# Kernel optimization log

Hardware: AMD Instinct MI355X
Metric: run time of the kernel (lower is better)

The kernel has to match this reference:

```python
import jax, jax.numpy as jnp
import numpy as np

ALPHA = 0.5
INV_COEFF = 25.0
STD_COEFF = 25.0
COV_COEFF = 1.0
NUM_MATCHES = 50
EPS = 1e-5
GAMMA = 1.0


def _cdist(a, b):
    # (B,M,C),(B,N,C) -> (B,M,N) euclidean, matmul-based like torch.cdist
    a2 = jnp.sum(a * a, axis=-1, keepdims=True)            # (B,M,1)
    b2 = jnp.sum(b * b, axis=-1, keepdims=True)            # (B,N,1)
    d2 = a2 + jnp.swapaxes(b2, -1, -2) - 2.0 * jnp.einsum('bmc,bnc->bmn', a, b)
    return jnp.sqrt(jnp.maximum(d2, 0.0))


def _nn_match(input_maps, candidate_maps, distances, num_matches):
    # topk(k=1, largest=False) == min/argmin over last dim
    nn_dists = jnp.min(distances, axis=-1)                 # (B,M)
    nn_indices = jnp.argmin(distances, axis=-1)            # (B,M)
    # k smallest nn_dists, ascending order
    _, best_input_idx = jax.lax.top_k(-nn_dists, num_matches)   # (B,k)
    best_cand_idx = jnp.take_along_axis(nn_indices, best_input_idx, axis=1)
    filt_in = jnp.take_along_axis(input_maps, best_input_idx[:, :, None], axis=1)
    filt_cand = jnp.take_along_axis(candidate_maps, best_cand_idx[:, :, None], axis=1)
    return filt_in, filt_cand


def _off_diag_sq_sum(c):
    return jnp.sum(c * c) - jnp.sum(jnp.diag(c) ** 2)


def _std_term(x_flat):
    # unbiased variance over sample dim (torch var default)
    std = jnp.sqrt(jnp.var(x_flat, axis=0, ddof=1) + EPS)
    return jnp.mean(jax.nn.relu(GAMMA - std)) / 2.0


def _cov_term(x_flat):
    n, c = x_flat.shape
    xc = x_flat - jnp.mean(x_flat, axis=0)
    cov = xc.T @ xc / (n - 1)
    return _off_diag_sq_sum(cov) / c


def _vicreg_global(x, y):
    inv = jnp.mean((x - y) ** 2)
    std = _std_term(x) + _std_term(y)
    cov = _cov_term(x) + _cov_term(y)
    return INV_COEFF * inv + STD_COEFF * std + COV_COEFF * cov


def _vicregl_maps(x, y):
    # x, y: (B, k, C)
    inv = jnp.mean((x - y) ** 2)
    xf = x.reshape(-1, x.shape[-1])
    yf = y.reshape(-1, y.shape[-1])
    std = _std_term(xf) + _std_term(yf)
    cov = _cov_term(xf) + _cov_term(yf)
    return INV_COEFF * inv, STD_COEFF * std, COV_COEFF * cov


def _local_loss(spatial_1, spatial_2):
    B, C, H, W = spatial_1.shape
    maps_1 = spatial_1.reshape(B, C, H * W).transpose(0, 2, 1)   # (B,HW,C)
    maps_2 = spatial_2.reshape(B, C, H * W).transpose(0, 2, 1)
    d12 = _cdist(maps_1, maps_2)
    m1f, m1n = _nn_match(maps_1, maps_2, d12, NUM_MATCHES)
    d21 = _cdist(maps_2, maps_1)
    m2f, m2n = _nn_match(maps_2, maps_1, d21, NUM_MATCHES)
    inv1, var1, cov1 = _vicregl_maps(m1f, m1n)
    inv2, var2, cov2 = _vicregl_maps(m2f, m2n)
    return (inv1 + inv2) / 2 + (var1 + var2) / 2 + (cov1 + cov2) / 2


def setup_inputs() -> dict:
    key = jax.random.key(0)
    k1, k2, k3, k4 = jax.random.split(key, 4)
    B, C, H, W = 64, 768, 24, 24
    return {
        'spatial_1': jax.random.normal(k1, (B, C, H, W), dtype=jnp.float32),
        'pooled_1': jax.random.normal(k2, (B, C), dtype=jnp.float32),
        'spatial_2': jax.random.normal(k3, (B, C, H, W), dtype=jnp.float32),
        'pooled_2': jax.random.normal(k4, (B, C), dtype=jnp.float32),
    }


def reference(spatial_1, pooled_1, spatial_2, pooled_2):
    global_loss = _vicreg_global(pooled_1, pooled_2)
    local_loss = _local_loss(spatial_1, spatial_2)
    return ALPHA * global_loss + (1.0 - ALPHA) * local_loss
```

## Files before the change

### kernel.cpp

```cpp
#include <hip/hip_runtime.h>
#include <stdint.h>

typedef unsigned long long ull;
typedef unsigned int uint;
typedef unsigned short ushort;

typedef __attribute__((ext_vector_type(8))) short short8;
typedef __attribute__((ext_vector_type(4))) float floatx4;

#define B   64
#define C   768
#define HW  576
#define K   50
#define NLOC (B*K)

#define OFF_SLOTS   0
#define OFF_COLSUM  256
#define OFF_NN1     18688
#define OFF_NN2     313600
#define OFF_SELP    608512
#define OFF_SELQ    634112
#define OFF_XT      954624
#define OFF_MP      OFF_XT
#define OFF_XGT     114200832
#define OFF_M       133861632

#define SLOT_INVG 0
#define SLOT_STD  1
#define SLOT_COV  7
#define SLOT_INV1 13
#define SLOT_INV2 14

__device__ __forceinline__ ull umin64(ull a, ull b) { return a < b ? a : b; }

__device__ __forceinline__ float bf2f_lo(uint u) { return __uint_as_float(u << 16); }
__device__ __forceinline__ float bf2f_hi(uint u) { return __uint_as_float(u & 0xffff0000u); }
__device__ __forceinline__ float bf2f(ushort u) { return __uint_as_float(((uint)u) << 16); }

__device__ __forceinline__ ushort f2bf(float f) {
    uint u = __float_as_uint(f);
    uint r = (u + 0x7fffu + ((u >> 16) & 1u)) >> 16;
    return (ushort)r;
}

__device__ __forceinline__ float blk_reduce_sum(float v, float* s4) {
    for (int off = 32; off > 0; off >>= 1) v += __shfl_down(v, off, 64);
    int lane = threadIdx.x & 63, w = threadIdx.x >> 6;
    if (lane == 0) s4[w] = v;
    __syncthreads();
    float r = 0.f;
    if (threadIdx.x == 0) r = s4[0] + s4[1] + s4[2] + s4[3];
    return r;
}

__global__ __launch_bounds__(256) void convert_kernel(const float* __restrict__ x1,
                                                      const float* __restrict__ x2,
                                                      ushort* __restrict__ xT,
                                                      float* __restrict__ normp) {
    int z = blockIdx.y;
    int which = z >> 6, b = z & 63;
    int half = blockIdx.x & 1;
    int pt = blockIdx.x >> 1;
    int p0 = pt * 64, c0 = half * 384;
    const float* X = (which ? x2 : x1) + ((size_t)b * C + c0) * HW + p0;

    __shared__ ushort tile[64][392];
    __shared__ float nlds[64][4];

    int t = threadIdx.x;
    int pq = t & 15, cq = t >> 4;
    int w = t >> 6;

    float ss[4] = {0.f, 0.f, 0.f, 0.f};

#pragma unroll
    for (int pass = 0; pass < 6; ++pass) {
        floatx4 v[4];
#pragma unroll
        for (int i = 0; i < 4; ++i)
            v[i] = *(const floatx4*)(X + (size_t)(pass * 64 + 4 * cq + i) * HW + 4 * pq);
#pragma unroll
        for (int j = 0; j < 4; ++j) {
            ushort u0 = f2bf(v[0][j]), u1 = f2bf(v[1][j]);
            ushort u2 = f2bf(v[2][j]), u3 = f2bf(v[3][j]);
            ushort4 uu; uu.x = u0; uu.y = u1; uu.z = u2; uu.w = u3;
            *(ushort4*)&tile[4 * pq + j][pass * 64 + 4 * cq] = uu;
            float r0 = bf2f(u0), r1 = bf2f(u1), r2 = bf2f(u2), r3 = bf2f(u3);
            ss[j] = fmaf(r0, r0, ss[j]); ss[j] = fmaf(r1, r1, ss[j]);
            ss[j] = fmaf(r2, r2, ss[j]); ss[j] = fmaf(r3, r3, ss[j]);
        }
    }
#pragma unroll
    for (int j = 0; j < 4; ++j) {
        ss[j] += __shfl_xor(ss[j], 16, 64);
        ss[j] += __shfl_xor(ss[j], 32, 64);
    }
    if ((t & 63) < 16) {
#pragma unroll
        for (int j = 0; j < 4; ++j) nlds[4 * pq + j][w] = ss[j];
    }
    __syncthreads();

    ushort* dst = xT + (((size_t)which * B + b) * HW + p0) * C + c0;
    const char* tb = (const char*)tile;
#pragma unroll
    for (int step = 0; step < 12; ++step) {
        int ib = (step * 256 + t) * 16;
        int p = ib / 768, cb = ib % 768;
        short8 vv = *(const short8*)(tb + (size_t)p * 784 + cb);
        *(short8*)(dst + (size_t)p * C + (cb >> 1)) = vv;
    }
    if (t < 64) {
        float nv = nlds[t][0] + nlds[t][1] + nlds[t][2] + nlds[t][3];
        normp[((size_t)half * 128 + which * 64 + b) * HW + p0 + t] = nv;
    }
}

template<int NG>
__device__ __forceinline__ void gemm_pp64(const ushort* gA, const ushort* gB0, const ushort* gB1,
                                          char* pool, int w,
                                          const int (&offA)[4], const int (&offB)[2],
                                          floatx4 (&acc)[4][2]) {
    auto issue = [&](int h) {
        char* buf = pool + (h & 3) * 12288;
        __builtin_amdgcn_global_load_lds(
            (const __attribute__((address_space(1))) void*)(gA + h * 32),
            (__attribute__((address_space(3))) void*)(buf + w * 1024), 16, 0, 0);
        __builtin_amdgcn_global_load_lds(
            (const __attribute__((address_space(1))) void*)(gB0 + h * 32),
            (__attribute__((address_space(3))) void*)(buf + 4096 + w * 1024), 16, 0, 0);
        __builtin_amdgcn_global_load_lds(
            (const __attribute__((address_space(1))) void*)(gB1 + h * 32),
            (__attribute__((address_space(3))) void*)(buf + 4096 + (4 + w) * 1024), 16, 0, 0);
    };
    issue(0); issue(1); issue(2);
    for (int h = 0; h < NG; ++h) {
        if (h < NG - 2)       asm volatile("s_waitcnt vmcnt(6)" ::: "memory");
        else if (h == NG - 2) asm volatile("s_waitcnt vmcnt(3)" ::: "memory");
        else                  asm volatile("s_waitcnt vmcnt(0)" ::: "memory");
        __builtin_amdgcn_s_barrier();
        if (h + 3 < NG) issue(h + 3);
        __builtin_amdgcn_sched_barrier(0);
        const char* buf = pool + (h & 3) * 12288;
        short8 a[4], bb[2];
#pragma unroll
        for (int i = 0; i < 4; ++i) a[i] = *(const short8*)(buf + offA[i]);
#pragma unroll
        for (int j = 0; j < 2; ++j) bb[j] = *(const short8*)(buf + offB[j]);
#pragma unroll
        for (int i = 0; i < 4; ++i)
#pragma unroll
            for (int j = 0; j < 2; ++j)
                acc[i][j] = __builtin_amdgcn_mfma_f32_16x16x32_bf16(a[i], bb[j], acc[i][j], 0, 0, 0);
    }
}

__global__ __launch_bounds__(256, 3) void cdist_mfma(const ushort* __restrict__ xT,
                                                     const float* __restrict__ normp,
                                                     ull* __restrict__ nn1,
                                                     ull* __restrict__ nn2) {
    int id = blockIdx.x;
    int xcd = id & 7, slot = id >> 3;
    int b = xcd + 8 * (slot / 45);
    int t = slot % 45;
    int qt = t % 5, pt = t / 5;

    const ushort* X1 = xT + (size_t)b * HW * C;
    const ushort* X2 = xT + (size_t)(B + b) * HW * C;

    __shared__ ull pool[6144];
    char* poolc = (char*)pool;

    int tid = threadIdx.x;
    int w = tid >> 6, l = tid & 63;
    int quad = l >> 4, col = l & 15;
    int lrow = l >> 2, pos = l & 3;

    int smA = w * 16 + lrow;
    int cdatA = pos ^ ((smA >> 1) & 3);
    const ushort* gA = X1 + (size_t)(pt * 64 + smA) * C + cdatA * 8;
    int smB0 = w * 16 + lrow;
    int cdatB0 = pos ^ ((smB0 >> 1) & 3);
    int q0 = qt * 128 + smB0; if (q0 >= HW) q0 = HW - 1;
    const ushort* gB0 = X2 + (size_t)q0 * C + cdatB0 * 8;
    int smB1 = 64 + w * 16 + lrow;
    int cdatB1 = pos ^ ((smB1 >> 1) & 3);
    int q1 = qt * 128 + smB1; if (q1 >= HW) q1 = HW - 1;
    const ushort* gB1 = X2 + (size_t)q1 * C + cdatB1 * 8;

    int offA[4], offB[2];
#pragma unroll
    for (int i = 0; i < 4; ++i) {
        int p_loc = i * 16 + col;
        offA[i] = p_loc * 64 + ((quad ^ ((p_loc >> 1) & 3)) * 16);
    }
#pragma unroll
    for (int j = 0; j < 2; ++j) {
        int q_loc = w * 32 + j * 16 + col;
        offB[j] = 4096 + q_loc * 64 + ((quad ^ ((q_loc >> 1) & 3)) * 16);
    }

    floatx4 zero = {0.f, 0.f, 0.f, 0.f};
    floatx4 acc[4][2];
#pragma unroll
    for (int i = 0; i < 4; ++i)
#pragma unroll
        for (int j = 0; j < 2; ++j) acc[i][j] = zero;

    gemm_pp64<24>(gA, gB0, gB1, poolc, w, offA, offB, acc);

    const float* n1a = normp + (size_t)b * HW;
    const float* n1b = normp + (size_t)(128 + b) * HW;
    const float* n2a = normp + (size_t)(64 + b) * HW;
    const float* n2b = normp + (size_t)(192 + b) * HW;
    float n1v[4][4];
    float n2v[2]; bool vq[2]; int qg[2];
#pragma unroll
    for (int i = 0; i < 4; ++i)
#pragma unroll
        for (int r = 0; r < 4; ++r) {
            int p = pt * 64 + i * 16 + quad * 4 + r;
            n1v[i][r] = n1a[p] + n1b[p];
        }
#pragma unroll
    for (int j = 0; j < 2; ++j) {
        int q = qt * 128 + w * 32 + j * 16 + col;
        qg[j] = q;
        vq[j] = (q < HW);
        int qc = q < HW ? q : (HW - 1);
        n2v[j] = n2a[qc] + n2b[qc];
    }

    __syncthreads();
    typedef ull row65[65];
    row65* red = (row65*)pool;

#pragma unroll
    for (int i = 0; i < 4; ++i)
#pragma unroll
        for (int r = 0; r < 4; ++r) {
            int p_loc = i * 16 + quad * 4 + r;
            ull best = ~0ull;
#pragma unroll
            for (int j = 0; j < 2; ++j) {
                if (!vq[j]) continue;
                float d2 = fmaxf(n1v[i][r] + n2v[j] - 2.0f * acc[i][j][r], 0.0f);
                best = umin64(best, ((ull)__float_as_uint(d2) << 32) | (unsigned)qg[j]);
            }
            red[p_loc][w * 16 + col] = best;
        }
    __syncthreads();
    if (tid < 64) {
        ull m = ~0ull;
#pragma unroll
        for (int x = 0; x < 64; ++x) m = umin64(m, red[tid][x]);
        atomicMin(&nn1[(size_t)b * HW + pt * 64 + tid], m);
    }
#pragma unroll
    for (int j = 0; j < 2; ++j) {
        ull best = ~0ull;
#pragma unroll
        for (int i = 0; i < 4; ++i)
#pragma unroll
            for (int r = 0; r < 4; ++r) {
                float d2 = fmaxf(n1v[i][r] + n2v[j] - 2.0f * acc[i][j][r], 0.0f);
                unsigned p_glob = pt * 64 + i * 16 + quad * 4 + r;
                best = umin64(best, ((ull)__float_as_uint(d2) << 32) | p_glob);
            }
        best = umin64(best, __shfl_xor(best, 16, 64));
        best = umin64(best, __shfl_xor(best, 32, 64));
        if (quad == 0 && vq[j])
            atomicMin(&nn2[(size_t)b * HW + qg[j]], best);
    }
}

__global__ __launch_bounds__(64) void select_topk_wave(const ull* __restrict__ nn1,
                                                       const ull* __restrict__ nn2,
                                                       int* __restrict__ sel_p,
                                                       int* __restrict__ sel_q) {
    int b = blockIdx.x, dir = blockIdx.y;
    const ull* nn = dir ? nn2 : nn1;
    int lane = threadIdx.x;
    ull key[9]; uint qv[9];
#pragma unroll
    for (int r = 0; r < 9; ++r) {
        int p = r * 64 + lane;
        ull e = nn[(size_t)b * HW + p];
        key[r] = (e & 0xFFFFFFFF00000000ull) | (unsigned)p;
        qv[r] = (uint)(e & 0xFFFFFFFFu);
    }
    int* sp = sel_p + (dir * B + b) * K;
    int* sq = sel_q + (dir * B + b) * K;
    for (int it = 0; it < K; ++it) {
        ull m = key[0];
#pragma unroll
        for (int r = 1; r < 9; ++r) m = umin64(m, key[r]);
#pragma unroll
        for (int off = 32; off > 0; off >>= 1) m = umin64(m, __shfl_xor(m, off, 64));
#pragma unroll
        for (int r = 0; r < 9; ++r) {
            if (key[r] == m) {
                sp[it] = (int)(uint)(m & 0xFFFFFFFFu);
                sq[it] = (int)qv[r];
                key[r] = ~0ull;
            }
        }
    }
}

__global__ __launch_bounds__(256) void gather_jmajor(const ushort* __restrict__ xT,
                                                     const int* __restrict__ sel_p,
                                                     const int* __restrict__ sel_q,
                                                     ushort* __restrict__ XgT) {
    int j = blockIdx.x, s = blockIdx.y;
    int dir = s >> 1;
    int whichsrc = (s == 1 || s == 2) ? 1 : 0;
    const int* sel = (s & 1) ? sel_q : sel_p;
    __shared__ int sidx[64];
    __shared__ uint buf[64][33];
    int tid = threadIdx.x;
    if (tid < 64) sidx[tid] = sel[(dir * B + tid) * K + j];
    __syncthreads();
    int rb = tid >> 2, u = tid & 3;
    const ushort* srow = xT + (((size_t)whichsrc * B + rb) * HW + sidx[rb]) * C;
    int wv = tid >> 6, lb = tid & 63;
    ushort* obase = XgT + (size_t)s * C * NLOC + (size_t)j * 64 + lb;
    for (int ch = 0; ch < 12; ++ch) {
        __syncthreads();
        uint4 v0 = *(const uint4*)(srow + ch * 64 + u * 8);
        uint4 v1 = *(const uint4*)(srow + ch * 64 + (u + 4) * 8);
        buf[rb][u * 4 + 0] = v0.x; buf[rb][u * 4 + 1] = v0.y;
        buf[rb][u * 4 + 2] = v0.z; buf[rb][u * 4 + 3] = v0.w;
        buf[rb][(u + 4) * 4 + 0] = v1.x; buf[rb][(u + 4) * 4 + 1] = v1.y;
        buf[rb][(u + 4) * 4 + 2] = v1.z; buf[rb][(u + 4) * 4 + 3] = v1.w;
        __syncthreads();
#pragma unroll
        for (int st = 0; st < 16; ++st) {
            int cl = wv + st * 4;
            uint uv = buf[lb][cl >> 1];
            ushort val = (cl & 1) ? (ushort)(uv >> 16) : (ushort)(uv & 0xffffu);
            obase[(size_t)(ch * 64 + cl) * NLOC] = val;
        }
    }
}

__global__ __launch_bounds__(256, 3) void ata_mfma(const ushort* __restrict__ XgT,
                                                   float* __restrict__ Mp) {
    int bx = blockIdx.x;
    int mat = blockIdx.y, split = blockIdx.z;
    int rt = bx / 6, ct = bx % 6;
    const ushort* X = XgT + (size_t)mat * C * NLOC;

    __shared__ ull pool[6144];
    char* poolc = (char*)pool;

    int tid = threadIdx.x;
    int w = tid >> 6, l = tid & 63;
    int quad = l >> 4, col = l & 15;
    int lrow = l >> 2, pos = l & 3;

    int smA = w * 16 + lrow;
    int cdatA = pos ^ ((smA >> 1) & 3);
    const ushort* gA = X + (size_t)(rt * 64 + smA) * NLOC + split * 640 + cdatA * 8;
    int smB0 = w * 16 + lrow;
    int cdatB0 = pos ^ ((smB0 >> 1) & 3);
    const ushort* gB0 = X + (size_t)(ct * 128 + smB0) * NLOC + split * 640 + cdatB0 * 8;
    int smB1 = 64 + w * 16 + lrow;
    int cdatB1 = pos ^ ((smB1 >> 1) & 3);
    const ushort* gB1 = X + (size_t)(ct * 128 + smB1) * NLOC + split * 640 + cdatB1 * 8;

    int offA[4], offB[2];
#pragma unroll
    for (int i = 0; i < 4; ++i) {
        int p_loc = i * 16 + col;
        offA[i] = p_loc * 64 + ((quad ^ ((p_loc >> 1) & 3)) * 16);
    }
#pragma unroll
    for (int j = 0; j < 2; ++j) {
        int q_loc = w * 32 + j * 16 + col;
        offB[j] = 4096 + q_loc * 64 + ((quad ^ ((q_loc >> 1) & 3)) * 16);
    }

    floatx4 zero = {0.f, 0.f, 0.f, 0.f};
    floatx4 acc[4][2];
#pragma unroll
    for (int i = 0; i < 4; ++i)
#pragma unroll
        for (int j = 0; j < 2; ++j) acc[i][j] = zero;

    gemm_pp64<20>(gA, gB0, gB1, poolc, w, offA, offB, acc);

    float* Mo = Mp + (size_t)(mat * 5 + split) * C * C;
#pragma unroll
    for (int i = 0; i < 4; ++i)
#pragma unroll
        for (int j = 0; j < 2; ++j)
#pragma unroll
            for (int r = 0; r < 4; ++r) {
                int row = rt * 64 + i * 16 + quad * 4 + r;
                int cc  = ct * 128 + w * 32 + j * 16 + col;
                Mo[(size_t)row * C + cc] = acc[i][j][r];
            }
}

__global__ __launch_bounds__(256) void ata_pooled(const float* __restrict__ p1,
                                                  const float* __restrict__ p2,
                                                  float* __restrict__ M,
                                                  float* __restrict__ colsum) {
    int mat = 4 + blockIdx.z;
    const float* X = (mat == 4) ? p1 : p2;
    int n = B;
    float* Mo = M + (size_t)mat * C * C;
    int ct = blockIdx.x, rt = blockIdx.y;

    __shared__ float As[16][64];
    __shared__ float Bs[16][64];
    int tid = threadIdx.x;
    int tx = tid & 15, ty = tid >> 4;
    int lr = tid >> 4, lc = (tid & 15) * 4;

    float acc[4][4] = {};
    for (int k0 = 0; k0 < n; k0 += 16) {
        float4 av = *(const float4*)&X[(size_t)(k0 + lr) * C + rt * 64 + lc];
        float4 bv = *(const float4*)&X[(size_t)(k0 + lr) * C + ct * 64 + lc];
        __syncthreads();
        *(float4*)&As[lr][lc] = av;
        *(float4*)&Bs[lr][lc] = bv;
        __syncthreads();
#pragma unroll
        for (int kk = 0; kk < 16; ++kk) {
            float4 af = *(const float4*)&As[kk][ty * 4];
            float4 bf = *(const float4*)&Bs[kk][tx * 4];
            float a[4] = {af.x, af.y, af.z, af.w};
            float bb[4] = {bf.x, bf.y, bf.z, bf.w};
#pragma unroll
            for (int i = 0; i < 4; ++i)
#pragma unroll
                for (int j = 0; j < 4; ++j)
                    acc[i][j] = fmaf(a[i], bb[j], acc[i][j]);
        }
    }
#pragma unroll
    for (int i = 0; i < 4; ++i) {
        float4 o = {acc[i][0], acc[i][1], acc[i][2], acc[i][3]};
        *(float4*)&Mo[(size_t)(rt * 64 + ty * 4 + i) * C + ct * 64 + tx * 4] = o;
    }
    if (rt == 0 && tid < 64) {
        int c = ct * 64 + tid;
        float s = 0.f;
        for (int r = 0; r < B; ++r) s += X[(size_t)r * C + c];
        colsum[(size_t)mat * C + c] = s;
    }
}

__global__ __launch_bounds__(256) void xgt_scan(const ushort* __restrict__ XgT,
                                                float* __restrict__ colsum,
                                                float* __restrict__ slots) {
    int pair = blockIdx.y;
    int cb = blockIdx.x * 4;
    int r = threadIdx.x >> 6, lane = threadIdx.x & 63;
    int c = cb + r;
    const ushort* rowA = XgT + ((size_t)(2 * pair) * C + c) * NLOC;
    const ushort* rowB = XgT + ((size_t)(2 * pair + 1) * C + c) * NLOC;
    float sa = 0.f, sb = 0.f, sinv = 0.f;
    for (int k = 0; k < K; ++k) {
        int i = lane + 64 * k;
        float a = bf2f(rowA[i]);
        float b = bf2f(rowB[i]);
        sa += a;
        sb += b;
        float d = a - b;
        sinv = fmaf(d, d, sinv);
    }
    float ra = sa, rb = sb;
    for (int off = 32; off > 0; off >>= 1) {
        ra += __shfl_down(ra, off, 64);
        rb += __shfl_down(rb, off, 64);
    }
    if (lane == 0) {
        colsum[(2 * pair) * C + c] = ra;
        colsum[(2 * pair + 1) * C + c] = rb;
    }
    __shared__ float s4[4];
    float t = blk_reduce_sum(sinv, s4);
    if (threadIdx.x == 0) atomicAdd(&slots[(pair == 0) ? SLOT_INV1 : SLOT_INV2], t);
}

__global__ __launch_bounds__(256) void cov_kernel(const float* __restrict__ Mp,
                                                  const float* __restrict__ M,
                                                  const float* __restrict__ colsum,
                                                  float* __restrict__ slots) {
    int mat = blockIdx.y;
    float n = (mat < 4) ? (float)NLOC : (float)B;
    float invn1 = 1.0f / (n - 1.0f);
    __shared__ float cs_s[C];
    for (int c = threadIdx.x; c < C; c += 256) cs_s[c] = colsum[mat * C + c];
    __syncthreads();
    float s = 0.f, s_std = 0.f;
    int r0 = blockIdx.x * 16;
    for (int r = 0; r < 16; ++r) {
        int row = r0 + r;
        float csr = cs_s[row] / n;
        if (mat < 4) {
            const float* Mr0 = Mp + (size_t)(mat * 5 + 0) * C * C + (size_t)row * C;
            const float* Mr1 = Mp + (size_t)(mat * 5 + 1) * C * C + (size_t)row * C;
            const float* Mr2 = Mp + (size_t)(mat * 5 + 2) * C * C + (size_t)row * C;
            const float* Mr3 = Mp + (size_t)(mat * 5 + 3) * C * C + (size_t)row * C;
            const float* Mr4 = Mp + (size_t)(mat * 5 + 4) * C * C + (size_t)row * C;
            for (int c = threadIdx.x; c < C; c += 256) {
                float v = Mr0[c];
                v += Mr1[c]; v += Mr2[c]; v += Mr3[c]; v += Mr4[c];
                if (c != row) {
                    float cv = (v - csr * cs_s[c]) * invn1;
                    s = fmaf(cv, cv, s);
                } else {
                    float cs = cs_s[row];
                    float var = (v - cs * cs / n) / (n - 1.0f);
                    float sd = sqrtf(var + 1e-5f);
                    float g = 1.0f - sd;
                    s_std += (g > 0.f) ? g : 0.f;
                }
            }
        } else {
            const float* Mr = M + (size_t)mat * C * C + (size_t)row * C;
            for (int c = threadIdx.x; c < C; c += 256) {
                float v = Mr[c];
                if (c != row) {
                    float cv = (v - csr * cs_s[c]) * invn1;
                    s = fmaf(cv, cv, s);
                } else {
                    float cs = cs_s[row];
                    float var = (v - cs * cs / n) / (n - 1.0f);
                    float sd = sqrtf(var + 1e-5f);
                    float g = 1.0f - sd;
                    s_std += (g > 0.f) ? g : 0.f;
                }
            }
        }
    }
    __shared__ float s4[4];
    float t = blk_reduce_sum(s, s4);
    if (threadIdx.x == 0) atomicAdd(&slots[SLOT_COV + mat], t);
    __syncthreads();
    float t2 = blk_reduce_sum(s_std, s4);
    if (threadIdx.x == 0) atomicAdd(&slots[SLOT_STD + mat], t2);
}

__global__ __launch_bounds__(256) void inv_global_kernel(const float* __restrict__ p1,
                                                         const float* __restrict__ p2,
                                                         float* __restrict__ slots) {
    int idx = blockIdx.x * 256 + threadIdx.x;
    int stride = gridDim.x * 256;
    float s = 0.f;
    for (int i = idx; i < B * C; i += stride) {
        float d = p1[i] - p2[i];
        s = fmaf(d, d, s);
    }
    __shared__ float s4[4];
    float t = blk_reduce_sum(s, s4);
    if (threadIdx.x == 0) atomicAdd(&slots[SLOT_INVG], t);
}

__global__ void final_kernel(const float* __restrict__ slots, float* __restrict__ out) {
    float std_t[6], cov_t[6];
    for (int m = 0; m < 6; ++m) {
        std_t[m] = slots[SLOT_STD + m] / (float)C * 0.5f;
        cov_t[m] = slots[SLOT_COV + m] / (float)C;
    }
    float inv_g = slots[SLOT_INVG] / (float)(B * C);
    float global_loss = 25.0f * inv_g + 25.0f * (std_t[4] + std_t[5]) + (cov_t[4] + cov_t[5]);
    float inv1 = 25.0f * slots[SLOT_INV1] / (float)(NLOC * C);
    float inv2 = 25.0f * slots[SLOT_INV2] / (float)(NLOC * C);
    float var1 = 25.0f * (std_t[0] + std_t[1]);
    float var2 = 25.0f * (std_t[2] + std_t[3]);
    float cov1 = cov_t[0] + cov_t[1];
    float cov2 = cov_t[2] + cov_t[3];
    float local_loss = (inv1 + inv2) * 0.5f + (var1 + var2) * 0.5f + (cov1 + cov2) * 0.5f;
    out[0] = 0.5f * global_loss + 0.5f * local_loss;
}

extern "C" void kernel_launch(void* const* d_in, const int* in_sizes, int n_in,
                              void* d_out, int out_size, void* d_ws, size_t ws_size,
                              hipStream_t stream) {
    const float* spatial_1 = (const float*)d_in[0];
    const float* pooled_1  = (const float*)d_in[1];
    const float* spatial_2 = (const float*)d_in[2];
    const float* pooled_2  = (const float*)d_in[3];
    float* out = (float*)d_out;

    char* ws = (char*)d_ws;
    float*  slots  = (float*)(ws + OFF_SLOTS);
    float*  colsum = (float*)(ws + OFF_COLSUM);
    ull*    nn1    = (ull*)(ws + OFF_NN1);
    ull*    nn2    = (ull*)(ws + OFF_NN2);
    int*    sel_p  = (int*)(ws + OFF_SELP);
    int*    sel_q  = (int*)(ws + OFF_SELQ);
    ushort* xT     = (ushort*)(ws + OFF_XT);
    float*  Mp     = (float*)(ws + OFF_MP);
    ushort* XgT    = (ushort*)(ws + OFF_XGT);
    float*  M      = (float*)(ws + OFF_M);
    float*  normp  = (float*)(ws + OFF_M);

    hipMemsetAsync(ws, 0, OFF_NN1, stream);
    hipMemsetAsync(ws + OFF_NN1, 0xFF, OFF_SELP - OFF_NN1, stream);

    convert_kernel<<<dim3(18, 128), 256, 0, stream>>>(spatial_1, spatial_2, xT, normp);
    cdist_mfma<<<2880, 256, 0, stream>>>(xT, normp, nn1, nn2);
    select_topk_wave<<<dim3(B, 2), 64, 0, stream>>>(nn1, nn2, sel_p, sel_q);
    gather_jmajor<<<dim3(K, 4), 256, 0, stream>>>(xT, sel_p, sel_q, XgT);
    ata_mfma<<<dim3(72, 4, 5), 256, 0, stream>>>(XgT, Mp);
    ata_pooled<<<dim3(12, 12, 2), 256, 0, stream>>>(pooled_1, pooled_2, M, colsum);
    xgt_scan<<<dim3(192, 2), 256, 0, stream>>>(XgT, colsum, slots);
    cov_kernel<<<dim3(48, 6), 256, 0, stream>>>(Mp, M, colsum, slots);
    inv_global_kernel<<<dim3(96), 256, 0, stream>>>(pooled_1, pooled_2, slots);
    final_kernel<<<1, 1, 0, stream>>>(slots, out);
}
```

Baseline: 448.1 us.

## Exploit covariance symmetry, widen gather stores, fold global invariance into pooled kernel

The Gram-matrix kernel now computes only the upper-triangular 64x128 tiles, using 47 tiles instead of 72 and 4 K-splits of 800 instead of 5 of 640. The covariance reduction sums only the strictly upper triangle and doubles it, with row pairing to balance the work. The gather kernel writes packed 32-bit pairs instead of 16-bit scalars, and the global invariance sum moves into ata_pooled so one launch is removed. Together these cut MFMA work, partial-matrix traffic and launch overhead. The cost is some tile load imbalance, and correctness now relies on the triangular tile mapping covering every needed entry.

Result: faster. 436.8 us (-2.5%).

```diff
diff --git a/kernel.cpp b/kernel.cpp
--- a/kernel.cpp
+++ b/kernel.cpp
@@ -323,8 +323,10 @@
     __syncthreads();
     int rb = tid >> 2, u = tid & 3;
     const ushort* srow = xT + (((size_t)whichsrc * B + rb) * HW + sidx[rb]) * C;
-    int wv = tid >> 6, lb = tid & 63;
-    ushort* obase = XgT + (size_t)s * C * NLOC + (size_t)j * 64 + lb;
+    int wv = tid >> 6;
+    int half32 = (tid >> 5) & 1;
+    int lb2 = tid & 31;
+    ushort* obase0 = XgT + (size_t)s * C * NLOC + (size_t)j * 64;
     for (int ch = 0; ch < 12; ++ch) {
         __syncthreads();
         uint4 v0 = *(const uint4*)(srow + ch * 64 + u * 8);
@@ -335,11 +337,14 @@
         buf[rb][(u + 4) * 4 + 2] = v1.z; buf[rb][(u + 4) * 4 + 3] = v1.w;
         __syncthreads();
 #pragma unroll
-        for (int st = 0; st < 16; ++st) {
-            int cl = wv + st * 4;
-            uint uv = buf[lb][cl >> 1];
-            ushort val = (cl & 1) ? (ushort)(uv >> 16) : (ushort)(uv & 0xffffu);
-            obase[(size_t)(ch * 64 + cl) * NLOC] = val;
+        for (int st = 0; st < 8; ++st) {
+            int cl = wv * 2 + half32 + st * 8;
+            uint uv0 = buf[2 * lb2][cl >> 1];
+            uint uv1 = buf[2 * lb2 + 1][cl >> 1];
+            ushort a = (cl & 1) ? (ushort)(uv0 >> 16) : (ushort)(uv0 & 0xffffu);
+            ushort b2 = (cl & 1) ? (ushort)(uv1 >> 16) : (ushort)(uv1 & 0xffffu);
+            uint wr = (uint)a | ((uint)b2 << 16);
+            *(uint*)(obase0 + (size_t)(ch * 64 + cl) * NLOC + 2 * lb2) = wr;
         }
     }
 }
@@ -348,7 +353,13 @@
                                                    float* __restrict__ Mp) {
     int bx = blockIdx.x;
     int mat = blockIdx.y, split = blockIdx.z;
-    int rt = bx / 6, ct = bx % 6;
+    int ct, rt;
+    if (bx < 3)       { ct = 0; rt = bx; }
+    else if (bx < 8)  { ct = 1; rt = bx - 3; }
+    else if (bx < 15) { ct = 2; rt = bx - 8; }
+    else if (bx < 24) { ct = 3; rt = bx - 15; }
+    else if (bx < 35) { ct = 4; rt = bx - 24; }
+    else              { ct = 5; rt = bx - 35; }
     const ushort* X = XgT + (size_t)mat * C * NLOC;
 
     __shared__ ull pool[6144];
@@ -361,13 +372,13 @@
 
     int smA = w * 16 + lrow;
     int cdatA = pos ^ ((smA >> 1) & 3);
-    const ushort* gA = X + (size_t)(rt * 64 + smA) * NLOC + split * 640 + cdatA * 8;
+    const ushort* gA = X + (size_t)(rt * 64 + smA) * NLOC + split * 800 + cdatA * 8;
     int smB0 = w * 16 + lrow;
     int cdatB0 = pos ^ ((smB0 >> 1) & 3);
-    const ushort* gB0 = X + (size_t)(ct * 128 + smB0) * NLOC + split * 640 + cdatB0 * 8;
+    const ushort* gB0 = X + (size_t)(ct * 128 + smB0) * NLOC + split * 800 + cdatB0 * 8;
     int smB1 = 64 + w * 16 + lrow;
     int cdatB1 = pos ^ ((smB1 >> 1) & 3);
-    const ushort* gB1 = X + (size_t)(ct * 128 + smB1) * NLOC + split * 640 + cdatB1 * 8;
+    const ushort* gB1 = X + (size_t)(ct * 128 + smB1) * NLOC + split * 800 + cdatB1 * 8;
 
     int offA[4], offB[2];
 #pragma unroll
@@ -388,9 +399,9 @@
 #pragma unroll
         for (int j = 0; j < 2; ++j) acc[i][j] = zero;
 
-    gemm_pp64<20>(gA, gB0, gB1, poolc, w, offA, offB, acc);
-
-    float* Mo = Mp + (size_t)(mat * 5 + split) * C * C;
+    gemm_pp64<25>(gA, gB0, gB1, poolc, w, offA, offB, acc);
+
+    float* Mo = Mp + (size_t)(mat * 4 + split) * C * C;
 #pragma unroll
     for (int i = 0; i < 4; ++i)
 #pragma unroll
@@ -406,7 +417,8 @@
 __global__ __launch_bounds__(256) void ata_pooled(const float* __restrict__ p1,
                                                   const float* __restrict__ p2,
                                                   float* __restrict__ M,
-                                                  float* __restrict__ colsum) {
+                                                  float* __restrict__ colsum,
+                                                  float* __restrict__ slots) {
     int mat = 4 + blockIdx.z;
     const float* X = (mat == 4) ? p1 : p2;
     int n = B;
@@ -450,6 +462,18 @@
         float s = 0.f;
         for (int r = 0; r < B; ++r) s += X[(size_t)r * C + c];
         colsum[(size_t)mat * C + c] = s;
+    }
+    if (blockIdx.z == 0 && rt == 0) {
+        int c = ct * 64 + (tid & 63);
+        int r0_ = tid >> 6;
+        float s = 0.f;
+        for (int r = r0_; r < B; r += 4) {
+            float d = p1[(size_t)r * C + c] - p2[(size_t)r * C + c];
+            s = fmaf(d, d, s);
+        }
+        __shared__ float s4b[4];
+        float t = blk_reduce_sum(s, s4b);
+        if (tid == 0) atomicAdd(&slots[SLOT_INVG], t);
     }
 }
 
@@ -497,68 +521,51 @@
     for (int c = threadIdx.x; c < C; c += 256) cs_s[c] = colsum[mat * C + c];
     __syncthreads();
     float s = 0.f, s_std = 0.f;
-    int r0 = blockIdx.x * 16;
-    for (int r = 0; r < 16; ++r) {
-        int row = r0 + r;
+    int bx = blockIdx.x;
+    for (int rr = 0; rr < 16; ++rr) {
+        int row = (rr < 8) ? (8 * bx + rr) : (768 - 8 * bx - 16 + rr);
         float csr = cs_s[row] / n;
         if (mat < 4) {
-            const float* Mr0 = Mp + (size_t)(mat * 5 + 0) * C * C + (size_t)row * C;
-            const float* Mr1 = Mp + (size_t)(mat * 5 + 1) * C * C + (size_t)row * C;
-            const float* Mr2 = Mp + (size_t)(mat * 5 + 2) * C * C + (size_t)row * C;
-            const float* Mr3 = Mp + (size_t)(mat * 5 + 3) * C * C + (size_t)row * C;
-            const float* Mr4 = Mp + (size_t)(mat * 5 + 4) * C * C + (size_t)row * C;
-            for (int c = threadIdx.x; c < C; c += 256) {
+            const float* Mr0 = Mp + (size_t)(mat * 4 + 0) * C * C + (size_t)row * C;
+            const float* Mr1 = Mp + (size_t)(mat * 4 + 1) * C * C + (size_t)row * C;
+            const float* Mr2 = Mp + (size_t)(mat * 4 + 2) * C * C + (size_t)row * C;
+            const float* Mr3 = Mp + (size_t)(mat * 4 + 3) * C * C + (size_t)row * C;
+            if (threadIdx.x == 0) {
+                float v = Mr0[row];
+                v += Mr1[row]; v += Mr2[row]; v += Mr3[row];
+                float cs = cs_s[row];
+                float var = (v - cs * cs / n) / (n - 1.0f);
+                float g = 1.0f - sqrtf(var + 1e-5f);
+                s_std += (g > 0.f) ? g : 0.f;
+            }
+            for (int c = row + 1 + threadIdx.x; c < C; c += 256) {
                 float v = Mr0[c];
-                v += Mr1[c]; v += Mr2[c]; v += Mr3[c]; v += Mr4[c];
-                if (c != row) {
-                    float cv = (v - csr * cs_s[c]) * invn1;
-                    s = fmaf(cv, cv, s);
-                } else {
-                    float cs = cs_s[row];
-                    float var = (v - cs * cs / n) / (n - 1.0f);
-                    float sd = sqrtf(var + 1e-5f);
-                    float g = 1.0f - sd;
-                    s_std += (g > 0.f) ? g : 0.f;
-                }
+                v += Mr1[c]; v += Mr2[c]; v += Mr3[c];
+                float cv = (v - csr * cs_s[c]) * invn1;
+                s = fmaf(cv, cv, s);
             }
         } else {
             const float* Mr = M + (size_t)mat * C * C + (size_t)row * C;
-            for (int c = threadIdx.x; c < C; c += 256) {
-                float v = Mr[c];
-                if (c != row) {
-                    float cv = (v - csr * cs_s[c]) * invn1;
-                    s = fmaf(cv, cv, s);
-                } else {
-                    float cs = cs_s[row];
-                    float var = (v - cs * cs / n) / (n - 1.0f);
-                    float sd = sqrtf(var + 1e-5f);
-                    float g = 1.0f - sd;
-                    s_std += (g > 0.f) ? g : 0.f;
-                }
-            }
-        }
-    }
+            if (threadIdx.x == 0) {
+                float v = Mr[row];
+                float cs = cs_s[row];
+                float var = (v - cs * cs / n) / (n - 1.0f);
+                float g = 1.0f - sqrtf(var + 1e-5f);
+                s_std += (g > 0.f) ? g : 0.f;
+            }
+            for (int c = row + 1 + threadIdx.x; c < C; c += 256) {
+                float cv = (Mr[c] - csr * cs_s[c]) * invn1;
+                s = fmaf(cv, cv, s);
+            }
+        }
+    }
+    s *= 2.0f;
     __shared__ float s4[4];
     float t = blk_reduce_sum(s, s4);
     if (threadIdx.x == 0) atomicAdd(&slots[SLOT_COV + mat], t);
     __syncthreads();
     float t2 = blk_reduce_sum(s_std, s4);
     if (threadIdx.x == 0) atomicAdd(&slots[SLOT_STD + mat], t2);
-}
-
-__global__ __launch_bounds__(256) void inv_global_kernel(const float* __restrict__ p1,
-                                                         const float* __restrict__ p2,
-                                                         float* __restrict__ slots) {
-    int idx = blockIdx.x * 256 + threadIdx.x;
-    int stride = gridDim.x * 256;
-    float s = 0.f;
-    for (int i = idx; i < B * C; i += stride) {
-        float d = p1[i] - p2[i];
-        s = fmaf(d, d, s);
-    }
-    __shared__ float s4[4];
-    float t = blk_reduce_sum(s, s4);
-    if (threadIdx.x == 0) atomicAdd(&slots[SLOT_INVG], t);
 }
 
 __global__ void final_kernel(const float* __restrict__ slots, float* __restrict__ out) {
@@ -608,10 +615,9 @@
     cdist_mfma<<<2880, 256, 0, stream>>>(xT, normp, nn1, nn2);
     select_topk_wave<<<dim3(B, 2), 64, 0, stream>>>(nn1, nn2, sel_p, sel_q);
     gather_jmajor<<<dim3(K, 4), 256, 0, stream>>>(xT, sel_p, sel_q, XgT);
-    ata_mfma<<<dim3(72, 4, 5), 256, 0, stream>>>(XgT, Mp);
-    ata_pooled<<<dim3(12, 12, 2), 256, 0, stream>>>(pooled_1, pooled_2, M, colsum);
+    ata_mfma<<<dim3(47, 4, 4), 256, 0, stream>>>(XgT, Mp);
+    ata_pooled<<<dim3(12, 12, 2), 256, 0, stream>>>(pooled_1, pooled_2, M, colsum, slots);
     xgt_scan<<<dim3(192, 2), 256, 0, stream>>>(XgT, colsum, slots);
     cov_kernel<<<dim3(48, 6), 256, 0, stream>>>(Mp, M, colsum, slots);
-    inv_global_kernel<<<dim3(96), 256, 0, stream>>>(pooled_1, pooled_2, slots);
     final_kernel<<<1, 1, 0, stream>>>(slots, out);
 }
```
